# Kernel optimization log

Hardware: AMD Instinct MI355X
Metric: run time of the kernel (lower is better)

The kernel has to match this reference:

```python
import jax, jax.numpy as jnp
from jax import lax
import numpy as np

N = 1024           # num_nodes
E = 32768          # edges per hop adjacency (avg degree 32)
EMB, HID, REP = 128, 64, 32
PATH_LENGTHS = (2, 3)


def _conv2d(x, w, b, pad):
    y = lax.conv_general_dilated(x, w, (1, 1), [(pad, pad), (pad, pad)],
                                 dimension_numbers=('NCHW', 'OIHW', 'NCHW'))
    return y + b[None, :, None, None]


def _tconv2d(x, w, b):
    # ConvTranspose2d(kernel=2, stride=2, pad=0) == conv with lhs_dilation=2, pad=1 (out = 2*in)
    y = lax.conv_general_dilated(x, w, (1, 1), [(1, 1), (1, 1)],
                                 lhs_dilation=(2, 2),
                                 dimension_numbers=('NCHW', 'OIHW', 'NCHW'))
    return y + b[None, :, None, None]


def _maxpool2(x):
    return lax.reduce_window(x, -jnp.inf, lax.max, (1, 1, 2, 2), (1, 1, 2, 2), 'VALID')


def _att_block(a, p):
    # ConvEncoder: conv->pool->conv->pool->tconv->tconv, relu/relu/relu/sigmoid
    h = jax.nn.relu(_conv2d(a, p[0], p[1], 1))
    h = _maxpool2(h)
    h = jax.nn.relu(_conv2d(h, p[2], p[3], 2))
    h = _maxpool2(h)
    h = jax.nn.relu(_tconv2d(h, p[4], p[5]))
    return jax.nn.sigmoid(_tconv2d(h, p[6], p[7]))


def _dense_gcn_norm(A):
    # add_remaining_self_loops(fill=1) + D^{-1/2} A D^{-1/2}; deg = row-sum (scatter_add over row)
    A = A + jnp.diag(jnp.where(jnp.diagonal(A) == 0, 1.0, 0.0).astype(A.dtype))
    deg = A.sum(axis=1)
    safe = jnp.where(deg > 0, deg, 1.0)
    dinv = jnp.where(deg > 0, lax.rsqrt(safe), 0.0)
    return dinv[:, None] * A * dinv[None, :]


def _edges_to_dense(e):
    # torch.sparse.FloatTensor(idx, ones).to_dense() sums duplicate edges
    return jnp.zeros((N, N), jnp.float32).at[e[0], e[1]].add(1.0)


def _path_transform(adjs, p):
    # adjs: [L, N, N] dense per-hop adjacencies of one meta-path
    att = _att_block(adjs[None], p)[0][:, :N, :N]
    attended = adjs * att
    M = jnp.eye(N, dtype=adjs.dtype)
    for i in range(adjs.shape[0]):  # fixed small loop over hops
        M = _dense_gcn_norm(M @ attended[i])
    return M


def _forward(x, p0, p1, w1, bias1, w2, bias2, e00, e01, e10, e11, e12):
    A0 = jnp.stack([_edges_to_dense(e00), _edges_to_dense(e01)])
    A1 = jnp.stack([_edges_to_dense(e10), _edges_to_dense(e11), _edges_to_dense(e12)])
    M0 = _path_transform(A0, p0)
    M1 = _path_transform(A1, p1)
    A = jnp.maximum(M0, M1)  # coalesce(op='max') over union; values are >= 0
    An = _dense_gcn_norm(A)  # GCNConv internal normalization (same for both layers)
    h = jax.nn.relu(An @ (x @ w1) + bias1)
    # dropout inactive (eval mode)
    return An @ (h @ w2) + bias2


def setup_inputs():
    key = jax.random.key(0)
    ks = iter(jax.random.split(key, 40))
    d = {}
    d['x'] = jax.random.normal(next(ks), (N, EMB), jnp.float32)
    d['mp0_e0'] = jax.random.randint(next(ks), (2, E), 0, N)
    d['mp0_e1'] = jax.random.randint(next(ks), (2, E), 0, N)
    d['mp1_e0'] = jax.random.randint(next(ks), (2, E), 0, N)
    d['mp1_e1'] = jax.random.randint(next(ks), (2, E), 0, N)
    d['mp1_e2'] = jax.random.randint(next(ks), (2, E), 0, N)
    for bi, L in enumerate(PATH_LENGTHS):
        pre = 'b%d_' % bi
        d[pre + 'c1w'] = jax.random.normal(next(ks), (16, L, 3, 3), jnp.float32) * 0.1
        d[pre + 'c1b'] = jnp.zeros((16,), jnp.float32)
        d[pre + 'c2w'] = jax.random.normal(next(ks), (4, 16, 3, 3), jnp.float32) * 0.1
        d[pre + 'c2b'] = jnp.zeros((4,), jnp.float32)
        d[pre + 't1w'] = jax.random.normal(next(ks), (16, 4, 2, 2), jnp.float32) * 0.1
        d[pre + 't1b'] = jnp.zeros((16,), jnp.float32)
        d[pre + 't2w'] = jax.random.normal(next(ks), (L, 16, 2, 2), jnp.float32) * 0.1
        d[pre + 't2b'] = jnp.zeros((L,), jnp.float32)
    d['w1'] = jax.random.normal(next(ks), (EMB, HID), jnp.float32) * (1.0 / np.sqrt(EMB)).astype(np.float32)
    d['bias1'] = jnp.zeros((HID,), jnp.float32)
    d['w2'] = jax.random.normal(next(ks), (HID, REP), jnp.float32) * (1.0 / np.sqrt(HID)).astype(np.float32)
    d['bias2'] = jnp.zeros((REP,), jnp.float32)
    return d


def reference(x, mp0_e0, mp0_e1, mp1_e0, mp1_e1, mp1_e2,
              b0_c1w, b0_c1b, b0_c2w, b0_c2b, b0_t1w, b0_t1b, b0_t2w, b0_t2b,
              b1_c1w, b1_c1b, b1_c2w, b1_c2b, b1_t1w, b1_t1b, b1_t2w, b1_t2b,
              w1, bias1, w2, bias2):
    p0 = (b0_c1w, b0_c1b, b0_c2w, b0_c2b, b0_t1w, b0_t1b, b0_t2w, b0_t2b)
    p1 = (b1_c1w, b1_c1b, b1_c2w, b1_c2b, b1_t1w, b1_t1b, b1_t2w, b1_t2b)
    return _forward(x, p0, p1, w1, bias1, w2, bias2,
                    mp0_e0, mp0_e1, mp1_e0, mp1_e1, mp1_e2)
```

## Files before the change

### kernel.cpp

```cpp
#include <hip/hip_runtime.h>
#include <math.h>

#define N 1024
#define NN (N*N)
#define NE 32768

#define OFF_A    ((size_t)0)
#define OFF_H10  ((size_t)(5*NN))
#define OFF_M0   ((size_t)(5*NN))
#define OFF_CSR  ((size_t)(7*NN))
#define OFF_BT   ((size_t)(9*NN))
#define OFF_M1   ((size_t)(10*NN))
#define OFF_AN   ((size_t)(11*NN))
#define OFF_H20  ((size_t)(13*NN))
#define OFF_H21  (OFF_H20 + 264196)
#define OFF_SC   (OFF_H21 + 264196)
#define SC_D0a 0
#define SC_F0a 1024
#define SC_D1a 2048
#define SC_F1a 3072
#define SC_D0b 4096
#define SC_F0b 5120
#define SC_D1b 6144
#define SC_F1b 7168
#define SC_D1c 8192
#define SC_F1c 9216
#define SC_D2  10240
#define SC_F2  11264
#define SC_DEG 12288
#define SC_DGV 13312
#define OFF_XW1  (OFF_SC + 14336)
#define OFF_HB   (OFF_XW1 + 65536)
#define OFF_HW2  (OFF_HB + 65536)

#define CSR_STRIDE 96
#define CSRF (1024 * CSR_STRIDE)
#define CSC_MAXT 80

__global__ void k_scatter5(const int* __restrict__ e0, const int* __restrict__ e1,
                           const int* __restrict__ e2, const int* __restrict__ e3,
                           const int* __restrict__ e4, float* __restrict__ A) {
  int g = blockIdx.x * 256 + threadIdx.x;
  int seg = g >> 15;
  int k = g & 32767;
  const int* e = (seg == 0) ? e0 : (seg == 1) ? e1 : (seg == 2) ? e2 : (seg == 3) ? e3 : e4;
  atomicAdd(&A[(size_t)seg * NN + (size_t)e[k] * N + e[NE + k]], 1.0f);
}

template<int L>
__device__ __forceinline__ void conv1_body(const float* __restrict__ A,
    const float* __restrict__ W, const float* __restrict__ Bn, float* __restrict__ out) {
  __shared__ float sIn[L][34][35];
  __shared__ float sW[16 * L * 9];
  __shared__ float sB[16];
  int tid = threadIdx.y * 16 + threadIdx.x;
  for (int i = tid; i < 16 * L * 9; i += 256) sW[i] = W[i];
  if (tid < 16) sB[tid] = Bn[tid];
  const int x0 = blockIdx.x * 32 - 1;
  const int y0 = blockIdx.y * 32 - 1;
  for (int idx = tid; idx < L * 34 * 34; idx += 256) {
    int l = idx / (34 * 34);
    int rem = idx - l * 34 * 34;
    int r = rem / 34, c = rem - r * 34;
    int iy = y0 + r, ix = x0 + c;
    sIn[l][r][c] = (iy >= 0 && iy < N && ix >= 0 && ix < N) ? A[(size_t)l * NN + (size_t)iy * N + ix] : 0.f;
  }
  __syncthreads();
  const int tx = threadIdx.x, ty = threadIdx.y;
  float p[L][4][4];
  #pragma unroll
  for (int l = 0; l < L; ++l)
    #pragma unroll
    for (int r = 0; r < 4; ++r)
      #pragma unroll
      for (int c = 0; c < 4; ++c)
        p[l][r][c] = sIn[l][2 * ty + r][2 * tx + c];
  const int ox = blockIdx.x * 16 + tx;
  const int oy = blockIdx.y * 16 + ty;
  for (int oc = 0; oc < 16; ++oc) {
    float wr[L * 9];
    #pragma unroll
    for (int t = 0; t < L * 9; ++t) wr[t] = sW[oc * L * 9 + t];
    float m = -1e30f;
    #pragma unroll
    for (int dy = 0; dy < 2; ++dy)
      #pragma unroll
      for (int dx = 0; dx < 2; ++dx) {
        float s = 0.f;
        #pragma unroll
        for (int l = 0; l < L; ++l)
          #pragma unroll
          for (int ky = 0; ky < 3; ++ky)
            #pragma unroll
            for (int kx = 0; kx < 3; ++kx)
              s = fmaf(p[l][dy + ky][dx + kx], wr[l * 9 + ky * 3 + kx], s);
        m = fmaxf(m, s);
      }
    out[(size_t)oc * 512 * 512 + (size_t)oy * 512 + ox] = fmaxf(m + sB[oc], 0.f);
  }
}

__global__ __launch_bounds__(256) void k_conv1_both(const float* __restrict__ Ab,
    const float* __restrict__ W0, const float* __restrict__ b0,
    const float* __restrict__ W1, const float* __restrict__ b1, float* __restrict__ H1b) {
  if (blockIdx.z == 0) conv1_body<2>(Ab, W0, b0, H1b);
  else                 conv1_body<3>(Ab + 2 * NN, W1, b1, H1b + 4 * NN);
}

__global__ __launch_bounds__(256) void k_conv2_both(const float* __restrict__ H1b,
    const float* __restrict__ W0, const float* __restrict__ b0,
    const float* __restrict__ W1, const float* __restrict__ b1,
    float* __restrict__ H2_0, float* __restrict__ H2_1) {
  const int z = blockIdx.z;
  const float* in = H1b + (size_t)z * 4 * NN;
  const float* W  = z ? W1 : W0;
  const float* Bn = z ? b1 : b0;
  float* out = z ? H2_1 : H2_0;
  __shared__ float sIn[2][4][36][37];
  __shared__ float sW[4 * 16 * 9];
  __shared__ float sB[4];
  int tid = threadIdx.y * 16 + threadIdx.x;
  for (int i = tid; i < 4 * 16 * 9; i += 256) sW[i] = W[i];
  if (tid < 4) sB[tid] = Bn[tid];
  const int x0 = blockIdx.x * 32 - 2;
  const int y0 = blockIdx.y * 32 - 2;
  const int tx = threadIdx.x, ty = threadIdx.y;

  auto stage = [&](int g, int buf) {
    for (int idx = tid; idx < 4 * 36 * 36; idx += 256) {
      int icl = idx / 1296;
      int rem = idx - icl * 1296;
      int r = rem / 36, c = rem - r * 36;
      int iy = y0 + r, ix = x0 + c;
      sIn[buf][icl][r][c] = (iy >= 0 && iy < 512 && ix >= 0 && ix < 512)
                            ? in[(size_t)(4 * g + icl) * 262144 + (size_t)iy * 512 + ix] : 0.f;
    }
  };

  float acc[4][2][2];
  #pragma unroll
  for (int oc = 0; oc < 4; ++oc)
    #pragma unroll
    for (int dy = 0; dy < 2; ++dy)
      #pragma unroll
      for (int dx = 0; dx < 2; ++dx) acc[oc][dy][dx] = 0.f;

  stage(0, 0);
  for (int g = 0; g < 4; ++g) {
    __syncthreads();
    if (g < 3) stage(g + 1, (g + 1) & 1);
    const int buf = g & 1;
    #pragma unroll
    for (int icl = 0; icl < 4; ++icl) {
      float p[4][4];
      #pragma unroll
      for (int r = 0; r < 4; ++r)
        #pragma unroll
        for (int c = 0; c < 4; ++c) p[r][c] = sIn[buf][icl][2 * ty + r][2 * tx + c];
      #pragma unroll
      for (int oc = 0; oc < 4; ++oc)
        #pragma unroll
        for (int ky = 0; ky < 3; ++ky)
          #pragma unroll
          for (int kx = 0; kx < 3; ++kx) {
            float w = sW[oc * 144 + (4 * g + icl) * 9 + ky * 3 + kx];
            #pragma unroll
            for (int dy = 0; dy < 2; ++dy)
              #pragma unroll
              for (int dx = 0; dx < 2; ++dx)
                acc[oc][dy][dx] = fmaf(p[dy + ky][dx + kx], w, acc[oc][dy][dx]);
          }
    }
  }
  const int ox = blockIdx.x * 16 + tx;
  const int oy = blockIdx.y * 16 + ty;
  if (ox < 257 && oy < 257) {
    #pragma unroll
    for (int oc = 0; oc < 4; ++oc) {
      float m = fmaxf(fmaxf(acc[oc][0][0], acc[oc][0][1]), fmaxf(acc[oc][1][0], acc[oc][1][1]));
      out[(size_t)oc * 66049 + (size_t)oy * 257 + ox] = fmaxf(m + sB[oc], 0.f);
    }
  }
}

__global__ __launch_bounds__(256) void k_tc_both(
    const float* __restrict__ H2_0, const float* __restrict__ H2_1,
    const float* __restrict__ t1w0, const float* __restrict__ t1b0,
    const float* __restrict__ t2w0, const float* __restrict__ t2b0,
    const float* __restrict__ t1w1, const float* __restrict__ t1b1,
    const float* __restrict__ t2w1, const float* __restrict__ t2b1,
    float* __restrict__ Ab) {
  const int z = blockIdx.z;
  const int L = 2 + z;
  const float* in  = z ? H2_1 : H2_0;
  const float* W1p = z ? t1w1 : t1w0;
  const float* B1p = z ? t1b1 : t1b0;
  const float* W2p = z ? t2w1 : t2w0;
  const float* B2p = z ? t2b1 : t2b0;
  float* A = Ab + (size_t)z * 2 * NN;
  __shared__ float sW1[256], sB1[16], sW2[192], sB2[3];
  int tid = threadIdx.y * 16 + threadIdx.x;
  sW1[tid] = W1p[tid];
  if (tid < 16) sB1[tid] = B1p[tid];
  for (int i = tid; i < L * 64; i += 256) sW2[i] = W2p[i];
  if (tid < L) sB2[tid] = B2p[tid];
  __syncthreads();
  const int n = blockIdx.x * 16 + threadIdx.x;
  const int m = blockIdx.y * 16 + threadIdx.y;
  const int p = m >> 1, q = n >> 1;
  const int f1y = 1 - (m & 1), f1x = 1 - (n & 1);
  float vin[4];
  #pragma unroll
  for (int ci = 0; ci < 4; ++ci) vin[ci] = in[(size_t)ci * 66049 + (size_t)p * 257 + q];
  float v[16];
  #pragma unroll
  for (int c = 0; c < 16; ++c) {
    float s = sB1[c];
    #pragma unroll
    for (int ci = 0; ci < 4; ++ci)
      s = fmaf(vin[ci], sW1[c * 16 + ci * 4 + f1y * 2 + f1x], s);
    v[c] = fmaxf(s, 0.f);
  }
  for (int l = 0; l < L; ++l) {
    #pragma unroll
    for (int dy = 0; dy < 2; ++dy)
      #pragma unroll
      for (int dx = 0; dx < 2; ++dx) {
        float s = sB2[l];
        #pragma unroll
        for (int c = 0; c < 16; ++c)
          s = fmaf(v[c], sW2[l * 64 + c * 4 + (1 - dy) * 2 + (1 - dx)], s);
        float sg = 1.f / (1.f + expf(-s));
        size_t idx = (size_t)l * NN + (size_t)(2 * m + dy) * N + (2 * n + dx);
        A[idx] *= sg;
      }
  }
}

__global__ __launch_bounds__(256) void k_extract(const float* __restrict__ Ab,
    int* __restrict__ gcol, float* __restrict__ gval, int* __restrict__ gcnt,
    int* __restrict__ crowT, float* __restrict__ cvalT, int* __restrict__ ccnt,
    float* __restrict__ DEGACC,
    float* __restrict__ D0a, float* __restrict__ F0a,
    float* __restrict__ D1a, float* __restrict__ F1a) {
  const int row = blockIdx.x;
  const int y = blockIdx.y;
  const float* base = Ab + (size_t)y * NN + (size_t)row * N;
  __shared__ int cnt;
  __shared__ float sdiag;
  __shared__ float red[4];
  if (threadIdx.x == 0) cnt = 0;
  __syncthreads();
  const int j4 = threadIdx.x;
  float4 v = ((const float4*)base)[j4];
  if (j4 == (row >> 2)) sdiag = ((const float*)&v)[row & 3];
  if (y == 4) {
    if (threadIdx.x == 0) DEGACC[row] = 0.f;
    #pragma unroll
    for (int t = 0; t < 4; ++t) {
      float x = ((const float*)&v)[t];
      if (x != 0.f) {
        int j = 4 * j4 + t;
        int p = atomicAdd(&ccnt[j], 1);
        if (p < CSC_MAXT) { crowT[p * 1024 + j] = row; cvalT[p * 1024 + j] = x; }
      }
    }
    return;
  }
  const size_t rb = ((size_t)y * 1024 + row) * CSR_STRIDE;
  #pragma unroll
  for (int t = 0; t < 4; ++t) {
    float x = ((const float*)&v)[t];
    if (x != 0.f) {
      int p = atomicAdd(&cnt, 1);
      if (p < CSR_STRIDE) { gcol[rb + p] = 4 * j4 + t; gval[rb + p] = x; }
    }
  }
  float s = v.x + v.y + v.z + v.w;
  #pragma unroll
  for (int o = 32; o > 0; o >>= 1) s += __shfl_down(s, o, 64);
  if ((threadIdx.x & 63) == 0) red[threadIdx.x >> 6] = s;
  __syncthreads();
  if (threadIdx.x == 0) {
    gcnt[(size_t)y * 1024 + row] = (cnt < CSR_STRIDE) ? cnt : CSR_STRIDE;
    if (y == 0 || y == 2) {
      float tot = red[0] + red[1] + red[2] + red[3];
      float fl = (sdiag == 0.f) ? 1.f : 0.f;
      float deg = tot + fl;
      float* D = (y == 0) ? D0a : D1a;
      float* F = (y == 0) ? F0a : F1a;
      D[row] = (deg > 0.f) ? (1.f / sqrtf(deg)) : 0.f;
      F[row] = fl;
    }
  }
}

__global__ __launch_bounds__(256) void k_spmm(
    const int* __restrict__ gcol, const float* __restrict__ gval, const int* __restrict__ gcnt,
    const float* __restrict__ D0a, const float* __restrict__ F0a,
    const float* __restrict__ D1a, const float* __restrict__ F1a,
    float* __restrict__ M0, float* __restrict__ BT,
    float* __restrict__ D0b, float* __restrict__ F0b,
    float* __restrict__ D1b, float* __restrict__ F1b) {
  const int row = blockIdx.x;
  const int y = blockIdx.y;
  const int lm = y * 2, rm = y * 2 + 1;
  const float* Da = y ? D1a : D0a;
  const float* Fa = y ? F1a : F0a;
  __shared__ __align__(16) float acc[1024];
  __shared__ int lcol[112];
  __shared__ float lw[112];
  __shared__ int lrc[112];
  __shared__ int cl;
  __shared__ float red[4];
  __shared__ float sdiag;
  ((float4*)acc)[threadIdx.x] = make_float4(0.f, 0.f, 0.f, 0.f);
  const float di = Da[row];
  const int cnt_l = gcnt[(size_t)lm * 1024 + row];
  const size_t lb = ((size_t)lm * 1024 + row) * CSR_STRIDE;
  if (threadIdx.x < cnt_l) {
    int k = gcol[lb + threadIdx.x];
    lcol[threadIdx.x] = k;
    lw[threadIdx.x] = di * gval[lb + threadIdx.x] * Da[k];
    lrc[threadIdx.x] = gcnt[(size_t)rm * 1024 + k];
  }
  if (threadIdx.x == 0) {
    int c = cnt_l;
    if (Fa[row] != 0.f) {
      lcol[c] = row; lw[c] = di * di; lrc[c] = gcnt[(size_t)rm * 1024 + row]; ++c;
    }
    cl = c;
  }
  __syncthreads();
  const int sub = threadIdx.x >> 5, lane = threadIdx.x & 31;
  const int cle = cl;
  for (int e = sub; e < cle; e += 8) {
    const int k = lcol[e];
    const float w = lw[e];
    const int rc = lrc[e];
    const size_t rbv = ((size_t)rm * 1024 + k) * CSR_STRIDE;
    for (int t = lane; t < rc; t += 32)
      atomicAdd(&acc[gcol[rbv + t]], w * gval[rbv + t]);
  }
  __syncthreads();
  float4 o = ((const float4*)acc)[threadIdx.x];
  float* C = y ? BT : M0;
  ((float4*)(C + (size_t)row * N))[threadIdx.x] = o;
  if (threadIdx.x == (row >> 2)) sdiag = ((const float*)&o)[row & 3];
  float s = o.x + o.y + o.z + o.w;
  #pragma unroll
  for (int off = 32; off > 0; off >>= 1) s += __shfl_down(s, off, 64);
  if ((threadIdx.x & 63) == 0) red[threadIdx.x >> 6] = s;
  __syncthreads();
  if (threadIdx.x == 0) {
    float tot = red[0] + red[1] + red[2] + red[3];
    float fl = (sdiag == 0.f) ? 1.f : 0.f;
    float deg = tot + fl;
    float* D = y ? D1b : D0b;
    float* F = y ? F1b : F0b;
    D[row] = (deg > 0.f) ? (1.f / sqrtf(deg)) : 0.f;
    F[row] = fl;
  }
}

__global__ __launch_bounds__(256) void k_spmm2(const float* __restrict__ BT,
    const float* __restrict__ D1b, const float* __restrict__ F1b,
    const int* __restrict__ crowT, const float* __restrict__ cvalT, const int* __restrict__ ccnt,
    float* __restrict__ M1, float* __restrict__ DEGACC, float* __restrict__ DIAGV) {
  const int g0 = blockIdx.x << 3;
  const int j  = (blockIdx.y << 8) + threadIdx.x;
  __shared__ float bt[1024 * 9];
  __shared__ float wsum[4][8];
  const int tid = threadIdx.x;
  for (int kq = 0; kq < 4; ++kq) {
    const int k = (kq << 8) + tid;
    const float dv = D1b[k];
    #pragma unroll
    for (int row = 0; row < 8; ++row)
      bt[k * 9 + row] = BT[(size_t)(g0 + row) * N + k] * dv;
  }
  __syncthreads();
  if (tid < 8) {
    const int gr = g0 + tid;
    bt[gr * 9 + tid] += F1b[gr] * D1b[gr];
  }
  __syncthreads();
  int cn = ccnt[j];
  cn = min(cn, CSC_MAXT);
  float o[8];
  #pragma unroll
  for (int row = 0; row < 8; ++row) o[row] = 0.f;
  for (int t = 0; t < cn; ++t) {
    const int   r = crowT[t * 1024 + j];
    const float v = cvalT[t * 1024 + j];
    const int rb = r * 9;
    #pragma unroll
    for (int row = 0; row < 8; ++row)
      o[row] = fmaf(bt[rb + row], v, o[row]);
  }
  #pragma unroll
  for (int row = 0; row < 8; ++row) o[row] *= D1b[g0 + row];
  #pragma unroll
  for (int row = 0; row < 8; ++row)
    M1[(size_t)(g0 + row) * N + j] = o[row];
  if ((unsigned)(j - g0) < 8u) DIAGV[j] = o[j - g0];
  #pragma unroll
  for (int row = 0; row < 8; ++row) {
    float s = o[row];
    #pragma unroll
    for (int off = 32; off > 0; off >>= 1) s += __shfl_down(s, off, 64);
    if ((tid & 63) == 0) wsum[tid >> 6][row] = s;
  }
  __syncthreads();
  if (tid < 8) {
    float p = wsum[0][tid] + wsum[1][tid] + wsum[2][tid] + wsum[3][tid];
    atomicAdd(&DEGACC[g0 + tid], p);
  }
}

__global__ void k_fin(const float* __restrict__ DEGACC, const float* __restrict__ DIAGV,
                      float* __restrict__ D1c, float* __restrict__ F1c) {
  const int row = blockIdx.x * 256 + threadIdx.x;
  const float fl = (DIAGV[row] == 0.f) ? 1.f : 0.f;
  const float deg = DEGACC[row] + fl;
  D1c[row] = (deg > 0.f) ? (1.f / sqrtf(deg)) : 0.f;
  F1c[row] = fl;
}

__global__ __launch_bounds__(256) void k_maxdeg(const float* __restrict__ M0,
    const float* __restrict__ d0, const float* __restrict__ f0,
    const float* __restrict__ M1, const float* __restrict__ d1, const float* __restrict__ f1,
    float* __restrict__ Aout, float* __restrict__ dinv2, float* __restrict__ dflg2) {
  const int row = blockIdx.x;
  const int j4 = threadIdx.x;
  const float r0 = d0[row], r1 = d1[row];
  const float fl0 = f0[row], fl1 = f1[row];
  float4 a = ((const float4*)(M0 + (size_t)row * N))[j4];
  float4 b = ((const float4*)(M1 + (size_t)row * N))[j4];
  const float4 c0 = ((const float4*)d0)[j4];
  const float4 c1 = ((const float4*)d1)[j4];
  int d = row - 4 * j4;
  if ((unsigned)d < 4u) { ((float*)&a)[d] += fl0; ((float*)&b)[d] += fl1; }
  float4 o;
  o.x = fmaxf(a.x * r0 * c0.x, b.x * r1 * c1.x);
  o.y = fmaxf(a.y * r0 * c0.y, b.y * r1 * c1.y);
  o.z = fmaxf(a.z * r0 * c0.z, b.z * r1 * c1.z);
  o.w = fmaxf(a.w * r0 * c0.w, b.w * r1 * c1.w);
  ((float4*)(Aout + (size_t)row * N))[j4] = o;
  __shared__ float sdiag;
  if ((unsigned)d < 4u) sdiag = ((float*)&o)[d];
  float s = o.x + o.y + o.z + o.w;
  #pragma unroll
  for (int off = 32; off > 0; off >>= 1) s += __shfl_down(s, off, 64);
  __shared__ float red[4];
  if ((threadIdx.x & 63) == 0) red[threadIdx.x >> 6] = s;
  __syncthreads();
  if (threadIdx.x == 0) {
    float tot = red[0] + red[1] + red[2] + red[3];
    float fl = (sdiag == 0.0f) ? 1.0f : 0.0f;
    float deg = tot + fl;
    dinv2[row] = (deg > 0.0f) ? (1.0f / sqrtf(deg)) : 0.0f;
    dflg2[row] = fl;
  }
}

template<int K, int NCOL, bool BIAS, bool RELU>
__global__ void k_mm_small(const float* __restrict__ A, const float* __restrict__ B,
                           const float* __restrict__ bias, float* __restrict__ out) {
  const int j = threadIdx.x;
  const int i = blockIdx.x * blockDim.y + threadIdx.y;
  const float* ar = A + (size_t)i * K;
  float acc = 0.f;
  #pragma unroll 8
  for (int k = 0; k < K; ++k) acc = fmaf(ar[k], B[(size_t)k * NCOL + j], acc);
  if (BIAS) acc += bias[j];
  if (RELU) acc = fmaxf(acc, 0.f);
  out[(size_t)i * NCOL + j] = acc;
}

template<int NCOL, bool RELU>
__global__ void k_an_mm(const float* __restrict__ BT, const float* __restrict__ dinv,
                        const float* __restrict__ dflg, const float* __restrict__ Bm,
                        const float* __restrict__ bias, float* __restrict__ out) {
  const int j = threadIdx.x;
  const int i = blockIdx.x * blockDim.y + threadIdx.y;
  const float di = dinv[i];
  const float* ar = BT + (size_t)i * N;
  float acc = 0.f;
  for (int k = 0; k < N; k += 4) {
    float4 a4 = *(const float4*)&ar[k];
    float4 d4 = *(const float4*)&dinv[k];
    acc = fmaf(a4.x * d4.x, Bm[(size_t)(k + 0) * NCOL + j], acc);
    acc = fmaf(a4.y * d4.y, Bm[(size_t)(k + 1) * NCOL + j], acc);
    acc = fmaf(a4.z * d4.z, Bm[(size_t)(k + 2) * NCOL + j], acc);
    acc = fmaf(a4.w * d4.w, Bm[(size_t)(k + 3) * NCOL + j], acc);
  }
  acc = fmaf(dflg[i] * dinv[i], Bm[(size_t)i * NCOL + j], acc);
  acc = fmaf(di, acc, bias[j]);
  if (RELU) acc = fmaxf(acc, 0.f);
  out[(size_t)i * NCOL + j] = acc;
}

extern "C" void kernel_launch(void* const* d_in, const int* in_sizes, int n_in,
                              void* d_out, int out_size, void* d_ws, size_t ws_size,
                              hipStream_t stream) {
  const float* x     = (const float*)d_in[0];
  const float* w1    = (const float*)d_in[22];
  const float* bias1 = (const float*)d_in[23];
  const float* w2    = (const float*)d_in[24];
  const float* bias2 = (const float*)d_in[25];
  float* out = (float*)d_out;
  float* ws  = (float*)d_ws;

  float* A    = ws + OFF_A;
  float* H1   = ws + OFF_H10;
  float* M0   = ws + OFF_M0;
  float* BT   = ws + OFF_BT;
  float* M1   = ws + OFF_M1;
  float* AN   = ws + OFF_AN;
  float* H2_0 = ws + OFF_H20;
  float* H2_1 = ws + OFF_H21;
  int*   gcol  = (int*)(ws + OFF_CSR);
  float* gval  = ws + OFF_CSR + (size_t)4 * CSRF;
  int*   gcnt  = (int*)(ws + OFF_CSR + (size_t)8 * CSRF);
  int*   crowT = (int*)(ws + OFF_CSR + (size_t)8 * CSRF + 4096);
  float* cvalT = ws + OFF_CSR + (size_t)8 * CSRF + 4096 + CSC_MAXT * 1024;
  int*   ccnt  = (int*)(ws + OFF_CSR + (size_t)8 * CSRF + 4096 + (size_t)2 * CSC_MAXT * 1024);
  float* SC   = ws + OFF_SC;
  float *D0a = SC + SC_D0a, *F0a = SC + SC_F0a, *D1a = SC + SC_D1a, *F1a = SC + SC_F1a;
  float *D0b = SC + SC_D0b, *F0b = SC + SC_F0b, *D1b = SC + SC_D1b, *F1b = SC + SC_F1b;
  float *D1c = SC + SC_D1c, *F1c = SC + SC_F1c, *D2 = SC + SC_D2, *F2 = SC + SC_F2;
  float *DEGACC = SC + SC_DEG, *DIAGV = SC + SC_DGV;
  float* XW1 = ws + OFF_XW1;
  float* HB  = ws + OFF_HB;
  float* HW2 = ws + OFF_HW2;

  hipMemsetAsync(A, 0, (size_t)5 * NN * sizeof(float), stream);

  dim3 b256(256), b16(16, 16);
  k_mm_small<128, 64, false, false><<<256, dim3(64, 4), 0, stream>>>(x, w1, nullptr, XW1);

  k_scatter5<<<640, b256, 0, stream>>>((const int*)d_in[1], (const int*)d_in[2],
                                       (const int*)d_in[3], (const int*)d_in[4],
                                       (const int*)d_in[5], A);

  k_conv1_both<<<dim3(32, 32, 2), b16, 0, stream>>>(A,
      (const float*)d_in[6], (const float*)d_in[7],
      (const float*)d_in[14], (const float*)d_in[15], H1);
  k_conv2_both<<<dim3(17, 17, 2), b16, 0, stream>>>(H1,
      (const float*)d_in[8], (const float*)d_in[9],
      (const float*)d_in[16], (const float*)d_in[17], H2_0, H2_1);
  k_tc_both<<<dim3(32, 32, 2), b16, 0, stream>>>(H2_0, H2_1,
      (const float*)d_in[10], (const float*)d_in[11],
      (const float*)d_in[12], (const float*)d_in[13],
      (const float*)d_in[18], (const float*)d_in[19],
      (const float*)d_in[20], (const float*)d_in[21], A);

  hipMemsetAsync(ccnt, 0, 1024 * sizeof(int), stream);

  k_extract<<<dim3(1024, 5), b256, 0, stream>>>(A, gcol, gval, gcnt,
      crowT, cvalT, ccnt, DEGACC, D0a, F0a, D1a, F1a);

  k_spmm<<<dim3(1024, 2), b256, 0, stream>>>(gcol, gval, gcnt,
      D0a, F0a, D1a, F1a, M0, BT, D0b, F0b, D1b, F1b);

  k_spmm2<<<dim3(128, 4), b256, 0, stream>>>(BT, D1b, F1b, crowT, cvalT, ccnt,
                                             M1, DEGACC, DIAGV);
  k_fin<<<4, b256, 0, stream>>>(DEGACC, DIAGV, D1c, F1c);

  k_maxdeg<<<1024, b256, 0, stream>>>(M0, D0b, F0b, M1, D1c, F1c, AN, D2, F2);

  k_an_mm<64, true><<<256, dim3(64, 4), 0, stream>>>(AN, D2, F2, XW1, bias1, HB);
  k_mm_small<64, 32, false, false><<<128, dim3(32, 8), 0, stream>>>(HB, w2, nullptr, HW2);
  k_an_mm<32, false><<<128, dim3(32, 8), 0, stream>>>(AN, D2, F2, HW2, bias2, out);
}
```

Before: 392.1 us.

## Retile conv1/conv2 so each thread computes two pooled outputs with vector LDS reads

Both the conv1 and conv2 kernels now give each thread two horizontally adjacent pooled outputs over a 32x16 output tile. Input rows are staged with a 68-float stride and read back as float4+float2 vectors, and conv1 writes its outputs as float2. Conv2 drops the double-buffered 4-channel staging and instead stages one channel at a time across 16 synchronised iterations. The aim is to cut LDS reads per FMA and the number of blocks, at the cost of more barriers and no overlap between loading and compute in conv2.

```diff
diff --git a/kernel.cpp b/kernel.cpp
--- a/kernel.cpp
+++ b/kernel.cpp
@@ -49,43 +49,48 @@
 
 template<int L>
 __device__ __forceinline__ void conv1_body(const float* __restrict__ A,
-    const float* __restrict__ W, const float* __restrict__ Bn, float* __restrict__ out) {
-  __shared__ float sIn[L][34][35];
-  __shared__ float sW[16 * L * 9];
-  __shared__ float sB[16];
-  int tid = threadIdx.y * 16 + threadIdx.x;
+    const float* __restrict__ W, const float* __restrict__ Bn, float* __restrict__ out,
+    float* __restrict__ smem) {
+  float* sIn = smem;
+  float* sW  = smem + L * 34 * 68;
+  float* sB  = sW + 16 * L * 9;
+  const int tid = threadIdx.x;
   for (int i = tid; i < 16 * L * 9; i += 256) sW[i] = W[i];
   if (tid < 16) sB[tid] = Bn[tid];
-  const int x0 = blockIdx.x * 32 - 1;
-  const int y0 = blockIdx.y * 32 - 1;
-  for (int idx = tid; idx < L * 34 * 34; idx += 256) {
-    int l = idx / (34 * 34);
-    int rem = idx - l * 34 * 34;
-    int r = rem / 34, c = rem - r * 34;
-    int iy = y0 + r, ix = x0 + c;
-    sIn[l][r][c] = (iy >= 0 && iy < N && ix >= 0 && ix < N) ? A[(size_t)l * NN + (size_t)iy * N + ix] : 0.f;
-  }
-  __syncthreads();
-  const int tx = threadIdx.x, ty = threadIdx.y;
-  float p[L][4][4];
-  #pragma unroll
+  const int px0 = blockIdx.x * 32;
+  const int py0 = blockIdx.y * 16;
+  const int x0 = 2 * px0 - 1;
+  const int y0 = 2 * py0 - 1;
   for (int l = 0; l < L; ++l)
-    #pragma unroll
-    for (int r = 0; r < 4; ++r)
-      #pragma unroll
-      for (int c = 0; c < 4; ++c)
-        p[l][r][c] = sIn[l][2 * ty + r][2 * tx + c];
-  const int ox = blockIdx.x * 16 + tx;
-  const int oy = blockIdx.y * 16 + ty;
+    for (int idx = tid; idx < 34 * 68; idx += 256) {
+      int r = idx / 68, c = idx - r * 68;
+      int iy = y0 + r, ix = x0 + c;
+      sIn[(l * 34 + r) * 68 + c] = (c < 66 && iy >= 0 && iy < N && ix >= 0 && ix < N)
+                                   ? A[(size_t)l * NN + (size_t)iy * N + ix] : 0.f;
+    }
+  __syncthreads();
+  const int tx = tid & 15, ty = tid >> 4;
+  float p[L][4][6];
+  #pragma unroll
+  for (int l = 0; l < L; ++l)
+    #pragma unroll
+    for (int r = 0; r < 4; ++r) {
+      const float* src = &sIn[((l * 34) + (2 * ty + r)) * 68 + 4 * tx];
+      float4 a = *(const float4*)src;
+      float2 b = *(const float2*)(src + 4);
+      p[l][r][0] = a.x; p[l][r][1] = a.y; p[l][r][2] = a.z; p[l][r][3] = a.w;
+      p[l][r][4] = b.x; p[l][r][5] = b.y;
+    }
+  const size_t obase = (size_t)(py0 + ty) * 512 + px0 + 2 * tx;
   for (int oc = 0; oc < 16; ++oc) {
     float wr[L * 9];
     #pragma unroll
     for (int t = 0; t < L * 9; ++t) wr[t] = sW[oc * L * 9 + t];
-    float m = -1e30f;
+    float m0 = -1e30f, m1 = -1e30f;
     #pragma unroll
     for (int dy = 0; dy < 2; ++dy)
       #pragma unroll
-      for (int dx = 0; dx < 2; ++dx) {
+      for (int dxp = 0; dxp < 4; ++dxp) {
         float s = 0.f;
         #pragma unroll
         for (int l = 0; l < L; ++l)
@@ -93,18 +98,22 @@
           for (int ky = 0; ky < 3; ++ky)
             #pragma unroll
             for (int kx = 0; kx < 3; ++kx)
-              s = fmaf(p[l][dy + ky][dx + kx], wr[l * 9 + ky * 3 + kx], s);
-        m = fmaxf(m, s);
+              s = fmaf(p[l][dy + ky][dxp + kx], wr[l * 9 + ky * 3 + kx], s);
+        if (dxp < 2) m0 = fmaxf(m0, s); else m1 = fmaxf(m1, s);
       }
-    out[(size_t)oc * 512 * 512 + (size_t)oy * 512 + ox] = fmaxf(m + sB[oc], 0.f);
+    float2 o2;
+    o2.x = fmaxf(m0 + sB[oc], 0.f);
+    o2.y = fmaxf(m1 + sB[oc], 0.f);
+    *(float2*)&out[(size_t)oc * 262144 + obase] = o2;
   }
 }
 
 __global__ __launch_bounds__(256) void k_conv1_both(const float* __restrict__ Ab,
     const float* __restrict__ W0, const float* __restrict__ b0,
     const float* __restrict__ W1, const float* __restrict__ b1, float* __restrict__ H1b) {
-  if (blockIdx.z == 0) conv1_body<2>(Ab, W0, b0, H1b);
-  else                 conv1_body<3>(Ab + 2 * NN, W1, b1, H1b + 4 * NN);
+  __shared__ float smem[3 * 34 * 68 + 16 * 3 * 9 + 16];
+  if (blockIdx.z == 0) conv1_body<2>(Ab, W0, b0, H1b, smem);
+  else                 conv1_body<3>(Ab + 2 * NN, W1, b1, H1b + 4 * NN, smem);
 }
 
 __global__ __launch_bounds__(256) void k_conv2_both(const float* __restrict__ H1b,
@@ -116,69 +125,70 @@
   const float* W  = z ? W1 : W0;
   const float* Bn = z ? b1 : b0;
   float* out = z ? H2_1 : H2_0;
-  __shared__ float sIn[2][4][36][37];
+  __shared__ float sIn[36 * 68];
   __shared__ float sW[4 * 16 * 9];
   __shared__ float sB[4];
-  int tid = threadIdx.y * 16 + threadIdx.x;
+  const int tid = threadIdx.x;
   for (int i = tid; i < 4 * 16 * 9; i += 256) sW[i] = W[i];
   if (tid < 4) sB[tid] = Bn[tid];
-  const int x0 = blockIdx.x * 32 - 2;
-  const int y0 = blockIdx.y * 32 - 2;
-  const int tx = threadIdx.x, ty = threadIdx.y;
-
-  auto stage = [&](int g, int buf) {
-    for (int idx = tid; idx < 4 * 36 * 36; idx += 256) {
-      int icl = idx / 1296;
-      int rem = idx - icl * 1296;
-      int r = rem / 36, c = rem - r * 36;
-      int iy = y0 + r, ix = x0 + c;
-      sIn[buf][icl][r][c] = (iy >= 0 && iy < 512 && ix >= 0 && ix < 512)
-                            ? in[(size_t)(4 * g + icl) * 262144 + (size_t)iy * 512 + ix] : 0.f;
-    }
-  };
-
-  float acc[4][2][2];
+  const int px0 = blockIdx.x * 32;
+  const int py0 = blockIdx.y * 16;
+  const int x0 = 2 * px0 - 2;
+  const int y0 = 2 * py0 - 2;
+  const int tx = tid & 15, ty = tid >> 4;
+  float acc[4][2][4];
   #pragma unroll
   for (int oc = 0; oc < 4; ++oc)
     #pragma unroll
     for (int dy = 0; dy < 2; ++dy)
       #pragma unroll
-      for (int dx = 0; dx < 2; ++dx) acc[oc][dy][dx] = 0.f;
-
-  stage(0, 0);
-  for (int g = 0; g < 4; ++g) {
+      for (int dxp = 0; dxp < 4; ++dxp) acc[oc][dy][dxp] = 0.f;
+  for (int g = 0; g < 16; ++g) {
     __syncthreads();
-    if (g < 3) stage(g + 1, (g + 1) & 1);
-    const int buf = g & 1;
-    #pragma unroll
-    for (int icl = 0; icl < 4; ++icl) {
-      float p[4][4];
+    for (int idx = tid; idx < 36 * 68; idx += 256) {
+      int r = idx / 68, c = idx - r * 68;
+      int iy = y0 + r, ix = x0 + c;
+      sIn[r * 68 + c] = (c < 66 && iy >= 0 && iy < 512 && ix >= 0 && ix < 512)
+                        ? in[(size_t)g * 262144 + (size_t)iy * 512 + ix] : 0.f;
+    }
+    __syncthreads();
+    float q[4][6];
+    #pragma unroll
+    for (int r = 0; r < 4; ++r) {
+      const float* src = &sIn[(2 * ty + r) * 68 + 4 * tx];
+      float4 a = *(const float4*)src;
+      float2 b = *(const float2*)(src + 4);
+      q[r][0] = a.x; q[r][1] = a.y; q[r][2] = a.z; q[r][3] = a.w;
+      q[r][4] = b.x; q[r][5] = b.y;
+    }
+    #pragma unroll
+    for (int oc = 0; oc < 4; ++oc) {
+      float wr[9];
       #pragma unroll
-      for (int r = 0; r < 4; ++r)
+      for (int t = 0; t < 9; ++t) wr[t] = sW[oc * 144 + g * 9 + t];
+      #pragma unroll
+      for (int dy = 0; dy < 2; ++dy)
         #pragma unroll
-        for (int c = 0; c < 4; ++c) p[r][c] = sIn[buf][icl][2 * ty + r][2 * tx + c];
-      #pragma unroll
-      for (int oc = 0; oc < 4; ++oc)
-        #pragma unroll
-        for (int ky = 0; ky < 3; ++ky)
+        for (int dxp = 0; dxp < 4; ++dxp) {
+          float s = acc[oc][dy][dxp];
           #pragma unroll
-          for (int kx = 0; kx < 3; ++kx) {
-            float w = sW[oc * 144 + (4 * g + icl) * 9 + ky * 3 + kx];
+          for (int ky = 0; ky < 3; ++ky)
             #pragma unroll
-            for (int dy = 0; dy < 2; ++dy)
-              #pragma unroll
-              for (int dx = 0; dx < 2; ++dx)
-                acc[oc][dy][dx] = fmaf(p[dy + ky][dx + kx], w, acc[oc][dy][dx]);
-          }
-    }
-  }
-  const int ox = blockIdx.x * 16 + tx;
-  const int oy = blockIdx.y * 16 + ty;
-  if (ox < 257 && oy < 257) {
+            for (int kx = 0; kx < 3; ++kx)
+              s = fmaf(q[dy + ky][dxp + kx], wr[ky * 3 + kx], s);
+          acc[oc][dy][dxp] = s;
+        }
+    }
+  }
+  const int oy = py0 + ty;
+  const int ox0 = px0 + 2 * tx;
+  if (oy < 257) {
     #pragma unroll
     for (int oc = 0; oc < 4; ++oc) {
-      float m = fmaxf(fmaxf(acc[oc][0][0], acc[oc][0][1]), fmaxf(acc[oc][1][0], acc[oc][1][1]));
-      out[(size_t)oc * 66049 + (size_t)oy * 257 + ox] = fmaxf(m + sB[oc], 0.f);
+      float m0 = fmaxf(fmaxf(acc[oc][0][0], acc[oc][0][1]), fmaxf(acc[oc][1][0], acc[oc][1][1]));
+      float m1 = fmaxf(fmaxf(acc[oc][0][2], acc[oc][0][3]), fmaxf(acc[oc][1][2], acc[oc][1][3]));
+      if (ox0 < 257)     out[(size_t)oc * 66049 + (size_t)oy * 257 + ox0]     = fmaxf(m0 + sB[oc], 0.f);
+      if (ox0 + 1 < 257) out[(size_t)oc * 66049 + (size_t)oy * 257 + ox0 + 1] = fmaxf(m1 + sB[oc], 0.f);
     }
   }
 }
@@ -544,10 +554,10 @@
                                        (const int*)d_in[3], (const int*)d_in[4],
                                        (const int*)d_in[5], A);
 
-  k_conv1_both<<<dim3(32, 32, 2), b16, 0, stream>>>(A,
+  k_conv1_both<<<dim3(16, 32, 2), b256, 0, stream>>>(A,
       (const float*)d_in[6], (const float*)d_in[7],
       (const float*)d_in[14], (const float*)d_in[15], H1);
-  k_conv2_both<<<dim3(17, 17, 2), b16, 0, stream>>>(H1,
+  k_conv2_both<<<dim3(9, 17, 2), b256, 0, stream>>>(H1,
       (const float*)d_in[8], (const float*)d_in[9],
       (const float*)d_in[16], (const float*)d_in[17], H2_0, H2_1);
   k_tc_both<<<dim3(32, 32, 2), b16, 0, stream>>>(H2_0, H2_1,
```

New measurement: 427.0 us. +8.9%, slower.
